# Kernel optimization log

Hardware: AMD Instinct MI355X
Metric: run time of the kernel (lower is better)

The kernel has to match this reference:

```python
import jax, jax.numpy as jnp
import numpy as np
from jax import lax

B, T = 64, 512
VOCAB, E = 16000, 128
USCRIPT, UE = 64, 16
F, MAX_NGRAM = 128, 5
C = 13  # num_classes


def setup_inputs() -> dict:
    key = jax.random.key(0)
    ks = jax.random.split(key, 18)
    inp = {
        "input_char": jax.random.randint(ks[0], (B, T), 0, VOCAB),
        "input_script": jax.random.randint(ks[1], (B, T), 0, USCRIPT),
        "input_mask": jnp.ones((B, T), dtype=bool),
        "char_emb": jax.random.normal(ks[2], (VOCAB, E), jnp.float32) * 0.02,
        "uscript_emb": jax.random.normal(ks[3], (USCRIPT, UE), jnp.float32) * 0.02,
        "dense_w": jax.random.normal(ks[4], (MAX_NGRAM * F + UE, C), jnp.float32) * 0.05,
        "dense_b": jnp.zeros((C,), jnp.float32),
        "trans": jax.random.normal(ks[5], (C, C), jnp.float32) * 0.1,
        "left_b": jax.random.normal(ks[6], (C,), jnp.float32) * 0.1,
        "right_b": jax.random.normal(ks[7], (C,), jnp.float32) * 0.1,
    }
    for i in range(1, MAX_NGRAM + 1):
        inp[f"conv_w{i}"] = jax.random.normal(ks[7 + i], (i, E, F), jnp.float32) * (1.0 / np.sqrt(i * E))
        inp[f"conv_b{i}"] = jnp.zeros((F,), jnp.float32)
    return inp


def _conv1d_same_relu(x, w, b):
    # x: [B,T,Cin], w: [K,Cin,Cout]
    y = lax.conv_general_dilated(x, w, window_strides=(1,), padding="SAME",
                                 dimension_numbers=("NWC", "WIO", "NWC"))
    return jax.nn.relu(y + b)


def _potentials(input_char, input_script, input_mask, char_emb, uscript_emb,
                conv_ws, conv_bs, dense_w, dense_b, left_b, right_b):
    emb = char_emb[input_char]              # [B,T,E]
    uemb = uscript_emb[input_script]        # [B,T,UE]
    feats = [_conv1d_same_relu(emb, w, b) for w, b in zip(conv_ws, conv_bs)]
    ctx = jnp.concatenate(feats + [uemb], axis=-1)          # [B,T,5F+UE]
    pot = jnp.einsum("btf,fc->btc", ctx, dense_w) + dense_b  # [B,T,C]
    # boundary energies (tfa CRF use_boundary=True): add left_b at first
    # valid step, right_b at last valid step per the mask
    m = input_mask.astype(pot.dtype)[..., None]              # [B,T,1]
    prev_m = jnp.pad(m[:, :-1], ((0, 0), (1, 0), (0, 0)))
    next_m = jnp.pad(m[:, 1:], ((0, 0), (0, 1), (0, 0)))
    pot = pot + m * (1.0 - prev_m) * left_b + m * (1.0 - next_m) * right_b
    return pot


def _viterbi_decode(pot, trans):
    # pot: [B,T,C], trans: [C,C]; full-length sequences (mask all ones)
    def fwd(state, pot_t):
        scores = state[:, :, None] + trans[None]   # [B, prev, cur]
        bp = jnp.argmax(scores, axis=1)            # [B,C]
        state = jnp.max(scores, axis=1) + pot_t    # [B,C]
        return state, bp

    final, bps = lax.scan(fwd, pot[:, 0], jnp.swapaxes(pot[:, 1:], 0, 1))
    last = jnp.argmax(final, axis=-1)              # [B]

    def back(tag, bp_t):
        prev = jnp.take_along_axis(bp_t, tag[:, None], axis=1)[:, 0]
        return prev, prev

    _, tags = lax.scan(back, last, bps, reverse=True)  # [T-1, B], forward order
    decoded = jnp.concatenate([jnp.swapaxes(tags, 0, 1), last[:, None]], axis=1)
    return decoded.astype(jnp.int32)


def reference(input_char, input_script, input_mask, char_emb, uscript_emb,
              conv_w1, conv_b1, conv_w2, conv_b2, conv_w3, conv_b3,
              conv_w4, conv_b4, conv_w5, conv_b5,
              dense_w, dense_b, trans, left_b, right_b):
    conv_ws = [conv_w1, conv_w2, conv_w3, conv_w4, conv_w5]
    conv_bs = [conv_b1, conv_b2, conv_b3, conv_b4, conv_b5]
    pot = _potentials(input_char, input_script, input_mask, char_emb, uscript_emb,
                      conv_ws, conv_bs, dense_w, dense_b, left_b, right_b)
    seq_len = jnp.sum(input_mask.astype(jnp.int32), axis=1)
    decoded = _viterbi_decode(pot, trans)
    return decoded, pot, seq_len, trans
```

## Files before the change

kernel.cpp:

```cpp
#include <hip/hip_runtime.h>

#define NB 64
#define NT 512
#define NC 13
#define AP 136
#define WP 72
#define PT 516
#define USTRIDE 18432
#define DWT_H   552960
#define DWT_L   563200
#define WS_NEED 1146880
#define WS_SROWS 1146880
#define WS_NEED2 (WS_SROWS + NB*NT*16*4)

typedef short s8v __attribute__((ext_vector_type(8)));
typedef float f4v __attribute__((ext_vector_type(4)));
typedef unsigned short ush;
typedef unsigned int u32;

__device__ __forceinline__ ush f2bf(float f){
    union { float f; u32 u; } v; v.f = f;
    u32 r = v.u + 0x7fffu + ((v.u >> 16) & 1u);
    return (ush)(r >> 16);
}
__device__ __forceinline__ float bf2f(ush h){
    union { u32 u; float f; } v; v.u = ((u32)h) << 16; return v.f;
}

__global__ __launch_bounds__(512)
void prep_kernel(const float* __restrict__ cw1, const float* __restrict__ cw2,
                 const float* __restrict__ cw3, const float* __restrict__ cw4,
                 const float* __restrict__ cw5, const float* __restrict__ dense_w,
                 ush* __restrict__ ws)
{
    int bx = blockIdx.x, tid = threadIdx.x;
    if (bx < 30) {
        int u = bx, ut = u >> 1, eh = u & 1;
        int fb = ut<1?0: ut<3?1: ut<6?2: ut<10?3:4;
        int jj = ut - fb*(fb+1)/2;
        const float* cw = fb==0?cw1: fb==1?cw2: fb==2?cw3: fb==3?cw4: cw5;
        #pragma unroll
        for (int it = 0; it < 2; ++it) {
            int g = it*512 + tid;
            int f = g & 127;
            int e8 = (g >> 7) << 3;
            float v[8];
            #pragma unroll
            for (int q = 0; q < 8; ++q)
                v[q] = cw[(jj*128 + eh*64 + e8 + q)*128 + f];
            ush h8[8], l8[8];
            #pragma unroll
            for (int q = 0; q < 8; ++q) {
                h8[q] = f2bf(v[q]);
                l8[q] = f2bf(v[q] - bf2f(h8[q]));
            }
            uint4 hv, lv;
            hv.x = h8[0] | ((u32)h8[1]<<16); hv.y = h8[2] | ((u32)h8[3]<<16);
            hv.z = h8[4] | ((u32)h8[5]<<16); hv.w = h8[6] | ((u32)h8[7]<<16);
            lv.x = l8[0] | ((u32)l8[1]<<16); lv.y = l8[2] | ((u32)l8[3]<<16);
            lv.z = l8[4] | ((u32)l8[5]<<16); lv.w = l8[6] | ((u32)l8[7]<<16);
            *(uint4*)&ws[u*USTRIDE + f*WP + e8]        = hv;
            *(uint4*)&ws[u*USTRIDE + 9216 + f*WP + e8] = lv;
        }
    } else {
        int fb = bx - 30;
        #pragma unroll
        for (int it = 0; it < 4; ++it) {
            int idx = it*512 + tid;
            int c = idx >> 7, f = idx & 127;
            float v = (c < 13) ? dense_w[(fb*128 + f)*13 + c] : 0.f;
            ush hi = f2bf(v);
            ws[DWT_H + fb*2048 + idx] = hi;
            ws[DWT_L + fb*2048 + idx] = f2bf(v - bf2f(hi));
        }
    }
}

__global__ __launch_bounds__(512)
void pot_kernel_ws(const int* __restrict__ input_char,
                   const int* __restrict__ input_script,
                   const float* __restrict__ char_emb,
                   const float* __restrict__ uscript_emb,
                   const float* __restrict__ dense_w,
                   const float* __restrict__ dense_b,
                   const float* __restrict__ left_b,
                   const float* __restrict__ right_b,
                   const float* __restrict__ cb1, const float* __restrict__ cb2,
                   const float* __restrict__ cb3, const float* __restrict__ cb4,
                   const float* __restrict__ cb5,
                   const ush* __restrict__ ws,
                   float* __restrict__ out_pot)
{
    __shared__ __align__(16) ush smem[77280];
    ush* Ah     = smem;
    ush* Al     = smem + 17952;
    ush* feat_h = smem + 54336;
    ush* feat_l = smem + 63040;
    float* uebt = (float*)(smem + 72768);
    float* dwue = (float*)(smem + 76864);

    const int tid  = threadIdx.x;
    const int lane = tid & 63;
    const int wid  = tid >> 6;
    const int tg   = wid >> 2;
    const int fg   = wid & 3;
    const int lr   = lane & 15;
    const int lq   = lane >> 4;
    const int bb   = blockIdx.x >> 2;
    const int t0   = (blockIdx.x & 3) << 7;

    {
        const char* g = (const char*)ws;
        char* l = (char*)(smem + 35904);
        #pragma unroll
        for (int i = 0; i < 5; ++i) {
            int idx = wid + (i << 3);
            if (i < 4 || wid < 4)
                __builtin_amdgcn_global_load_lds(
                    (const __attribute__((address_space(1))) void*)(g + idx*1024 + lane*16),
                    (__attribute__((address_space(3))) void*)(l + idx*1024 + lane*16), 16, 0, 0);
        }
    }

    for (int i = tid; i < 132*16; i += 512) {
        int row = i >> 4, s = (i & 15) << 3;
        int t = t0 + row - 2;
        uint4 hv = {0,0,0,0}, lv = {0,0,0,0};
        if (t >= 0 && t < NT) {
            int ch = input_char[bb*NT + t];
            const float* src = char_emb + ch*128 + s;
            float4 x0 = *(const float4*)src;
            float4 x1 = *(const float4*)(src + 4);
            float fs[8] = {x0.x,x0.y,x0.z,x0.w,x1.x,x1.y,x1.z,x1.w};
            ush h[8], l[8];
            #pragma unroll
            for (int q = 0; q < 8; ++q) {
                h[q] = f2bf(fs[q]);
                l[q] = f2bf(fs[q] - bf2f(h[q]));
            }
            hv.x = h[0] | ((u32)h[1]<<16); hv.y = h[2] | ((u32)h[3]<<16);
            hv.z = h[4] | ((u32)h[5]<<16); hv.w = h[6] | ((u32)h[7]<<16);
            lv.x = l[0] | ((u32)l[1]<<16); lv.y = l[2] | ((u32)l[3]<<16);
            lv.z = l[4] | ((u32)l[5]<<16); lv.w = l[6] | ((u32)l[7]<<16);
        }
        *(uint4*)&Ah[row*AP + s] = hv;
        *(uint4*)&Al[row*AP + s] = lv;
    }
    for (int i = tid; i < 2048; i += 512) {
        int uu = i >> 7, tl = i & 127;
        uebt[uu*128 + tl] = uscript_emb[input_script[bb*NT + t0 + tl]*16 + uu];
    }
    if (tid < 208) dwue[tid] = dense_w[640*13 + tid];
    __syncthreads();

    const float* cbs[5] = {cb1, cb2, cb3, cb4, cb5};

    f4v cacc[4][2];
    #pragma unroll
    for (int mt = 0; mt < 4; ++mt)
        #pragma unroll
        for (int nt = 0; nt < 2; ++nt) cacc[mt][nt] = (f4v){0.f,0.f,0.f,0.f};
    f4v dacc = (f4v){0.f,0.f,0.f,0.f};

    #pragma unroll 1
    for (int u = 0; u < 30; ++u) {
        int ut  = u >> 1, eh = u & 1;
        int fb  = ut<1?0: ut<3?1: ut<6?2: ut<10?3:4;
        int jj  = ut - fb*(fb+1)/2;
        int jsh = (2 - (fb >> 1)) + jj;

        if (u < 29) {
            const char* g = (const char*)ws + (u + 1)*36864;
            char* l = (char*)(smem + (((u + 1) & 1) ? 54336 : 35904));
            #pragma unroll
            for (int i = 0; i < 5; ++i) {
                int idx = wid + (i << 3);
                if (i < 4 || wid < 4)
                    __builtin_amdgcn_global_load_lds(
                        (const __attribute__((address_space(1))) void*)(g + idx*1024 + lane*16),
                        (__attribute__((address_space(3))) void*)(l + idx*1024 + lane*16), 16, 0, 0);
            }
        }

        const ush* Wh = smem + ((u & 1) ? 54336 : 35904);
        const ush* Wl = Wh + 9216;
        #pragma unroll
        for (int kk = 0; kk < 2; ++kk) {
            int ko = kk*32 + (lq << 3);
            s8v bh[2], bl[2];
            #pragma unroll
            for (int nt = 0; nt < 2; ++nt) {
                int frow = fg*32 + nt*16 + lr;
                bh[nt] = *(const s8v*)&Wh[frow*WP + ko];
                bl[nt] = *(const s8v*)&Wl[frow*WP + ko];
            }
            #pragma unroll
            for (int mt = 0; mt < 4; ++mt) {
                int row = tg*64 + mt*16 + lr + jsh;
                int ai  = row*AP + eh*64 + ko;
                s8v ah = *(const s8v*)&Ah[ai];
                s8v al = *(const s8v*)&Al[ai];
                #pragma unroll
                for (int nt = 0; nt < 2; ++nt) {
                    cacc[mt][nt] = __builtin_amdgcn_mfma_f32_16x16x32_bf16(ah, bh[nt], cacc[mt][nt], 0,0,0);
                    cacc[mt][nt] = __builtin_amdgcn_mfma_f32_16x16x32_bf16(ah, bl[nt], cacc[mt][nt], 0,0,0);
                    cacc[mt][nt] = __builtin_amdgcn_mfma_f32_16x16x32_bf16(al, bh[nt], cacc[mt][nt], 0,0,0);
                }
            }
        }

        if (u == 1 || u == 5 || u == 11 || u == 19 || u == 29) {
            __syncthreads();
            float cbv0 = cbs[fb][fg*32 + lr];
            float cbv1 = cbs[fb][fg*32 + 16 + lr];

            #pragma unroll 1
            for (int h = 0; h < 2; ++h) {
                if (tg == h) {
                    #pragma unroll
                    for (int mt = 0; mt < 4; ++mt)
                        #pragma unroll
                        for (int nt = 0; nt < 2; ++nt)
                            #pragma unroll
                            for (int r = 0; r < 4; ++r) {
                                float v = fmaxf(cacc[mt][nt][r] + (nt ? cbv1 : cbv0), 0.f);
                                int rw = mt*16 + (lq << 2) + r;
                                int f  = fg*32 + nt*16 + lr;
                                ush hh = f2bf(v);
                                feat_h[rw*AP + f] = hh;
                                feat_l[rw*AP + f] = f2bf(v - bf2f(hh));
                            }
                }
                __syncthreads();
                if (tg == h) {
                    int trow = fg*16 + lr;
                    #pragma unroll
                    for (int kf = 0; kf < 4; ++kf) {
                        int f0 = kf*32 + (lq << 3);
                        s8v a2h = *(const s8v*)&ws[DWT_H + fb*2048 + lr*128 + f0];
                        s8v a2l = *(const s8v*)&ws[DWT_L + fb*2048 + lr*128 + f0];
                        s8v b2h = *(const s8v*)&feat_h[trow*AP + f0];
                        s8v b2l = *(const s8v*)&feat_l[trow*AP + f0];
                        dacc = __builtin_amdgcn_mfma_f32_16x16x32_bf16(a2h, b2h, dacc, 0,0,0);
                        dacc = __builtin_amdgcn_mfma_f32_16x16x32_bf16(a2h, b2l, dacc, 0,0,0);
                        dacc = __builtin_amdgcn_mfma_f32_16x16x32_bf16(a2l, b2h, dacc, 0,0,0);
                    }
                    if (fb == 4) {
                        int tloc  = tg*64 + fg*16 + lr;
                        int tglob = t0 + tloc;
                        float pc[4];
                        #pragma unroll
                        for (int r = 0; r < 4; ++r) pc[r] = dacc[r];
                        #pragma unroll
                        for (int uu = 0; uu < 16; ++uu) {
                            float uv = uebt[uu*128 + tloc];
                            #pragma unroll
                            for (int r = 0; r < 4; ++r) {
                                int c = (lq << 2) + r;
                                if (c < 13) pc[r] = fmaf(uv, dwue[uu*13 + c], pc[r]);
                            }
                        }
                        #pragma unroll
                        for (int r = 0; r < 4; ++r) {
                            int c = (lq << 2) + r;
                            if (c < 13) {
                                float v = pc[r] + dense_b[c];
                                if (tglob == 0)    v += left_b[c];
                                if (tglob == NT-1) v += right_b[c];
                                out_pot[(bb*NT + tglob)*13 + c] = v;
                            }
                        }
                    }
                }
                __syncthreads();
            }
            #pragma unroll
            for (int mt = 0; mt < 4; ++mt)
                #pragma unroll
                for (int nt = 0; nt < 2; ++nt) cacc[mt][nt] = (f4v){0.f,0.f,0.f,0.f};
        } else {
            __syncthreads();
        }
    }
}

__global__ __launch_bounds__(512)
void pot_kernel_fb(const int* __restrict__ input_char,
                   const int* __restrict__ input_script,
                   const float* __restrict__ char_emb,
                   const float* __restrict__ uscript_emb,
                   const float* __restrict__ dense_w,
                   const float* __restrict__ dense_b,
                   const float* __restrict__ left_b,
                   const float* __restrict__ right_b,
                   const float* __restrict__ cw1, const float* __restrict__ cb1,
                   const float* __restrict__ cw2, const float* __restrict__ cb2,
                   const float* __restrict__ cw3, const float* __restrict__ cb3,
                   const float* __restrict__ cw4, const float* __restrict__ cb4,
                   const float* __restrict__ cw5, const float* __restrict__ cb5,
                   float* __restrict__ out_pot)
{
    __shared__ __align__(16) ush smem[71744];
    ush* Ah     = smem;
    ush* Al     = smem + 17952;
    ush* Wh     = smem + 35904;
    ush* Wl     = smem + 45120;
    ush* feat_h = smem + 54336;
    ush* feat_l = smem + 63040;
    float* dwlds = (float*)(smem + 35904);
    float* dwue  = (float*)(smem + 39232);
    float* uebt  = (float*)(smem + 39648);

    const int tid  = threadIdx.x;
    const int lane = tid & 63;
    const int wid  = tid >> 6;
    const int tg   = wid >> 2;
    const int fg   = wid & 3;
    const int lr   = lane & 15;
    const int lq   = lane >> 4;
    const int bb   = blockIdx.x >> 2;
    const int t0   = (blockIdx.x & 3) << 7;

    for (int i = tid; i < 132*16; i += 512) {
        int row = i >> 4, s = (i & 15) << 3;
        int t = t0 + row - 2;
        uint4 hv = {0,0,0,0}, lv = {0,0,0,0};
        if (t >= 0 && t < NT) {
            int ch = input_char[bb*NT + t];
            const float* src = char_emb + ch*128 + s;
            float4 x0 = *(const float4*)src;
            float4 x1 = *(const float4*)(src + 4);
            float fs[8] = {x0.x,x0.y,x0.z,x0.w,x1.x,x1.y,x1.z,x1.w};
            ush h[8], l[8];
            #pragma unroll
            for (int q = 0; q < 8; ++q) {
                h[q] = f2bf(fs[q]);
                l[q] = f2bf(fs[q] - bf2f(h[q]));
            }
            hv.x = h[0] | ((u32)h[1]<<16); hv.y = h[2] | ((u32)h[3]<<16);
            hv.z = h[4] | ((u32)h[5]<<16); hv.w = h[6] | ((u32)h[7]<<16);
            lv.x = l[0] | ((u32)l[1]<<16); lv.y = l[2] | ((u32)l[3]<<16);
            lv.z = l[4] | ((u32)l[5]<<16); lv.w = l[6] | ((u32)l[7]<<16);
        }
        *(uint4*)&Ah[row*AP + s] = hv;
        *(uint4*)&Al[row*AP + s] = lv;
    }

    const float* cws[5] = {cw1, cw2, cw3, cw4, cw5};
    const float* cbs[5] = {cb1, cb2, cb3, cb4, cb5};

    f4v cacc[4][2];
    #pragma unroll
    for (int mt = 0; mt < 4; ++mt)
        #pragma unroll
        for (int nt = 0; nt < 2; ++nt) cacc[mt][nt] = (f4v){0.f,0.f,0.f,0.f};
    f4v dacc = (f4v){0.f,0.f,0.f,0.f};

    #pragma unroll 1
    for (int u = 0; u < 30; ++u) {
        int ut  = u >> 1, eh = u & 1;
        int fb  = ut<1?0: ut<3?1: ut<6?2: ut<10?3:4;
        int jj  = ut - fb*(fb+1)/2;
        int jsh = (2 - (fb >> 1)) + jj;
        const float* cw = cws[fb] + (jj*128 + eh*64)*128;

        __syncthreads();
        for (int g = tid; g < 1024; g += 512) {
            int f = g & 127, e8 = (g >> 7) << 3;
            float v[8];
            #pragma unroll
            for (int q = 0; q < 8; ++q) v[q] = cw[(e8 + q)*128 + f];
            ush h8[8], l8[8];
            #pragma unroll
            for (int q = 0; q < 8; ++q) {
                h8[q] = f2bf(v[q]);
                l8[q] = f2bf(v[q] - bf2f(h8[q]));
            }
            uint4 hv, lv;
            hv.x = h8[0] | ((u32)h8[1]<<16); hv.y = h8[2] | ((u32)h8[3]<<16);
            hv.z = h8[4] | ((u32)h8[5]<<16); hv.w = h8[6] | ((u32)h8[7]<<16);
            lv.x = l8[0] | ((u32)l8[1]<<16); lv.y = l8[2] | ((u32)l8[3]<<16);
            lv.z = l8[4] | ((u32)l8[5]<<16); lv.w = l8[6] | ((u32)l8[7]<<16);
            *(uint4*)&Wh[f*WP + e8] = hv;
            *(uint4*)&Wl[f*WP + e8] = lv;
        }
        __syncthreads();

        #pragma unroll
        for (int kk = 0; kk < 2; ++kk) {
            int ko = kk*32 + (lq << 3);
            s8v bh[2], bl[2];
            #pragma unroll
            for (int nt = 0; nt < 2; ++nt) {
                int frow = fg*32 + nt*16 + lr;
                bh[nt] = *(const s8v*)&Wh[frow*WP + ko];
                bl[nt] = *(const s8v*)&Wl[frow*WP + ko];
            }
            #pragma unroll
            for (int mt = 0; mt < 4; ++mt) {
                int row = tg*64 + mt*16 + lr + jsh;
                int ai  = row*AP + eh*64 + ko;
                s8v ah = *(const s8v*)&Ah[ai];
                s8v al = *(const s8v*)&Al[ai];
                #pragma unroll
                for (int nt = 0; nt < 2; ++nt) {
                    cacc[mt][nt] = __builtin_amdgcn_mfma_f32_16x16x32_bf16(ah, bh[nt], cacc[mt][nt], 0,0,0);
                    cacc[mt][nt] = __builtin_amdgcn_mfma_f32_16x16x32_bf16(ah, bl[nt], cacc[mt][nt], 0,0,0);
                    cacc[mt][nt] = __builtin_amdgcn_mfma_f32_16x16x32_bf16(al, bh[nt], cacc[mt][nt], 0,0,0);
                }
            }
        }

        if (u == 1 || u == 5 || u == 11 || u == 19 || u == 29) {
            __syncthreads();
            for (int i = tid; i < 128*13; i += 512)
                dwlds[i] = dense_w[fb*128*13 + i];
            if (fb == 4) {
                for (int i = tid; i < 16*13; i += 512)
                    dwue[i] = dense_w[640*13 + i];
                for (int i = tid; i < 2048; i += 512) {
                    int uu = i >> 7, tl = i & 127;
                    uebt[uu*128 + tl] = uscript_emb[input_script[bb*NT + t0 + tl]*16 + uu];
                }
            }
            __syncthreads();

            float cbv0 = cbs[fb][fg*32 + lr];
            float cbv1 = cbs[fb][fg*32 + 16 + lr];

            #pragma unroll 1
            for (int h = 0; h < 2; ++h) {
                if (tg == h) {
                    #pragma unroll
                    for (int mt = 0; mt < 4; ++mt)
                        #pragma unroll
                        for (int nt = 0; nt < 2; ++nt)
                            #pragma unroll
                            for (int r = 0; r < 4; ++r) {
                                float v = fmaxf(cacc[mt][nt][r] + (nt ? cbv1 : cbv0), 0.f);
                                int rw = mt*16 + (lq << 2) + r;
                                int f  = fg*32 + nt*16 + lr;
                                ush hh = f2bf(v);
                                feat_h[rw*AP + f] = hh;
                                feat_l[rw*AP + f] = f2bf(v - bf2f(hh));
                            }
                }
                __syncthreads();
                if (tg == h) {
                    int trow = fg*16 + lr;
                    #pragma unroll
                    for (int kf = 0; kf < 4; ++kf) {
                        int f0 = kf*32 + (lq << 3);
                        float dv[8];
                        #pragma unroll
                        for (int q = 0; q < 8; ++q) dv[q] = dwlds[(f0 + q)*13 + lr];
                        s8v a2h, a2l;
                        #pragma unroll
                        for (int q = 0; q < 8; ++q) {
                            ush hh = f2bf(dv[q]);
                            a2h[q] = (short)hh;
                            a2l[q] = (short)f2bf(dv[q] - bf2f(hh));
                        }
                        s8v b2h = *(const s8v*)&feat_h[trow*AP + f0];
                        s8v b2l = *(const s8v*)&feat_l[trow*AP + f0];
                        dacc = __builtin_amdgcn_mfma_f32_16x16x32_bf16(a2h, b2h, dacc, 0,0,0);
                        dacc = __builtin_amdgcn_mfma_f32_16x16x32_bf16(a2h, b2l, dacc, 0,0,0);
                        dacc = __builtin_amdgcn_mfma_f32_16x16x32_bf16(a2l, b2h, dacc, 0,0,0);
                    }
                    if (fb == 4) {
                        int tloc  = tg*64 + fg*16 + lr;
                        int tglob = t0 + tloc;
                        float pc[4];
                        #pragma unroll
                        for (int r = 0; r < 4; ++r) pc[r] = dacc[r];
                        #pragma unroll
                        for (int uu = 0; uu < 16; ++uu) {
                            float uv = uebt[uu*128 + tloc];
                            #pragma unroll
                            for (int r = 0; r < 4; ++r) {
                                int c = (lq << 2) + r;
                                if (c < 13) pc[r] = fmaf(uv, dwue[uu*13 + c], pc[r]);
                            }
                        }
                        #pragma unroll
                        for (int r = 0; r < 4; ++r) {
                            int c = (lq << 2) + r;
                            if (c < 13) {
                                float v = pc[r] + dense_b[c];
                                if (tglob == 0)    v += left_b[c];
                                if (tglob == NT-1) v += right_b[c];
                                out_pot[(bb*NT + tglob)*13 + c] = v;
                            }
                        }
                    }
                }
                __syncthreads();
            }
            #pragma unroll
            for (int mt = 0; mt < 4; ++mt)
                #pragma unroll
                for (int nt = 0; nt < 2; ++nt) cacc[mt][nt] = (f4v){0.f,0.f,0.f,0.f};
        }
    }
}

#define DPPF(dst, src, ctrl) \
    dst = __int_as_float(__builtin_amdgcn_mov_dpp(__float_as_int(src), ctrl, 0xF, 0xF, false))

__global__ __launch_bounds__(256)
void scan_kernel(const float* __restrict__ pot,
                 const float* __restrict__ trans,
                 float* __restrict__ srows)
{
    __shared__ __align__(16) float ptld[16 * PT];
    __shared__ float t_lds[NC * NC];

    const int b   = blockIdx.x;
    const int tid = threadIdx.x;

    for (int i = tid; i < 3 * PT; i += 256) ptld[13 * PT + i] = 0.f;
    for (int i = tid; i < NT * NC; i += 256) {
        int t = i / NC, c = i - t * NC;
        ptld[c * PT + t] = pot[b * NT * NC + i];
    }
    for (int i = tid; i < NC * NC; i += 256) t_lds[i] = trans[i];
    __syncthreads();

    if (tid >= 16) return;
    const int c = tid;
    int r1 = __builtin_amdgcn_mov_dpp(c, 0x121, 0xF, 0xF, false);
    const bool fwd = (r1 == ((c + 1) & 15));
    float tc[16];
    #pragma unroll
    for (int k = 0; k < 16; ++k) {
        int p = fwd ? ((c + k) & 15) : ((c - k) & 15);
        tc[k] = (c < 13 && p < 13) ? t_lds[p * NC + c] : -1e30f;
    }
    float s = (c < 13) ? ptld[c * PT] : -1e30f;
    float* srb = srows + b * NT * 16;
    srb[c] = s;
    int t = 1;

    auto step = [&](float pv) {
        float v0 = s, v1, v2, v3, v4, v5, v6, v7;
        float v8, v9, v10, v11, v12, v13, v14, v15;
        DPPF(v1, v0, 0x121);
        DPPF(v2, v0, 0x122); DPPF(v3, v1, 0x122);
        DPPF(v4, v0, 0x124); DPPF(v5, v1, 0x124);
        DPPF(v6, v2, 0x124); DPPF(v7, v3, 0x124);
        DPPF(v8,  v0, 0x128); DPPF(v9,  v1, 0x128);
        DPPF(v10, v2, 0x128); DPPF(v11, v3, 0x128);
        DPPF(v12, v4, 0x128); DPPF(v13, v5, 0x128);
        DPPF(v14, v6, 0x128); DPPF(v15, v7, 0x128);
        float m0 = fmaxf(v0  + tc[0],  v1  + tc[1]);
        float m1 = fmaxf(v2  + tc[2],  v3  + tc[3]);
        float m2 = fmaxf(v4  + tc[4],  v5  + tc[5]);
        float m3 = fmaxf(v6  + tc[6],  v7  + tc[7]);
        float m4 = fmaxf(v8  + tc[8],  v9  + tc[9]);
        float m5 = fmaxf(v10 + tc[10], v11 + tc[11]);
        float m6 = fmaxf(v12 + tc[12], v13 + tc[13]);
        float m7 = fmaxf(v14 + tc[14], v15 + tc[15]);
        float n0 = fmaxf(m0, m1), n1 = fmaxf(m2, m3);
        float n2 = fmaxf(m4, m5), n3 = fmaxf(m6, m7);
        s = fmaxf(fmaxf(n0, n1), fmaxf(n2, n3)) + pv;
        srb[t * 16 + c] = s;
        ++t;
    };

    const float* prow = &ptld[c * PT];
    float4 pvv = *(const float4*)&prow[4];
    step(prow[1]);
    step(prow[2]);
    step(prow[3]);
    #pragma unroll 1
    for (int t4 = 4; t4 < NT; t4 += 4) {
        float4 cur = pvv;
        if (t4 + 4 < NT) pvv = *(const float4*)&prow[t4 + 4];
        step(cur.x); step(cur.y); step(cur.z); step(cur.w);
    }
}

__global__ __launch_bounds__(256)
void backtrack_kernel(const float* __restrict__ srows,
                      const float* __restrict__ trans,
                      float* __restrict__ out_dec,
                      float* __restrict__ out_seq,
                      float* __restrict__ out_trans)
{
    __shared__ __align__(16) float sl[NT * 16];
    __shared__ float t_lds[NC * NC];
    __shared__ unsigned char path_lds[16 * 13 * 32];
    __shared__ unsigned char entry_lds[16 * 13];
    __shared__ int chunk_e[16];

    const int b   = blockIdx.x;
    const int tid = threadIdx.x;

    {
        const float4* src = reinterpret_cast<const float4*>(srows + b * NT * 16);
        float4* dst = reinterpret_cast<float4*>(sl);
        for (int i = tid; i < NT * 16 / 4; i += 256) dst[i] = src[i];
        for (int i = tid; i < NC * NC; i += 256) t_lds[i] = trans[i];
    }
    __syncthreads();

    if (tid < 16 * 13) {
        const int chunk = tid / 13;
        const int e     = tid - chunk * 13;
        unsigned char* path = &path_lds[(chunk * 13 + e) * 32];
        int cur = e;
        path[31] = (unsigned char)e;
        for (int tl = 31; tl >= 1; --tl) {
            const float* srow = &sl[(chunk * 32 + tl - 1) * 16];
            float best = -1e30f; int bi = 0;
            #pragma unroll
            for (int p = 0; p < NC; ++p) {
                float v = srow[p] + t_lds[p * NC + cur];
                if (v > best) { best = v; bi = p; }
            }
            cur = bi;
            path[tl - 1] = (unsigned char)cur;
        }
        if (chunk > 0) {
            const float* srow = &sl[(chunk * 32 - 1) * 16];
            float best = -1e30f; int bi = 0;
            #pragma unroll
            for (int p = 0; p < NC; ++p) {
                float v = srow[p] + t_lds[p * NC + cur];
                if (v > best) { best = v; bi = p; }
            }
            entry_lds[chunk * 13 + e] = (unsigned char)bi;
        }
    }
    __syncthreads();

    if (tid == 0) {
        float best = -1e30f; int last = 0;
        for (int c = 0; c < NC; ++c) {
            float v = sl[(NT - 1) * 16 + c];
            if (v > best) { best = v; last = c; }
        }
        chunk_e[15] = last;
        for (int i = 15; i >= 1; --i)
            chunk_e[i - 1] = entry_lds[i * 13 + chunk_e[i]];
    }
    __syncthreads();

    float* dec = out_dec + b * NT;
    for (int t = tid; t < NT; t += 256) {
        int ck = t >> 5;
        dec[t] = (float)path_lds[(ck * 13 + chunk_e[ck]) * 32 + (t & 31)];
    }
    if (tid == 0) out_seq[b] = (float)NT;
    if (b == 0) {
        for (int i = tid; i < NC * NC; i += 256) out_trans[i] = trans[i];
    }
}

__global__ __launch_bounds__(256)
void viterbi_mono(const float* __restrict__ pot,
                  const float* __restrict__ trans,
                  float* __restrict__ out_dec,
                  float* __restrict__ out_seq,
                  float* __restrict__ out_trans)
{
    __shared__ __align__(16) float s_lds[NT * NC];
    __shared__ __align__(16) float ptld[16 * PT];
    __shared__ float t_lds[NC * NC];
    __shared__ unsigned char path_lds[16 * 13 * 32];
    __shared__ unsigned char entry_lds[16 * 13];
    __shared__ int chunk_e[16];

    const int b   = blockIdx.x;
    const int tid = threadIdx.x;

    for (int i = tid; i < 3 * PT; i += 256) ptld[13 * PT + i] = 0.f;
    for (int i = tid; i < NT * NC; i += 256) {
        int t = i / NC, c = i - t * NC;
        float v = pot[b * NT * NC + i];
        ptld[c * PT + t] = v;
        if (t == 0) s_lds[c] = v;
    }
    for (int i = tid; i < NC * NC; i += 256) t_lds[i] = trans[i];
    __syncthreads();

    if (tid < 16) {
        const int c = tid;
        int r1 = __builtin_amdgcn_mov_dpp(c, 0x121, 0xF, 0xF, false);
        const bool fwd = (r1 == ((c + 1) & 15));
        float tc[16];
        #pragma unroll
        for (int k = 0; k < 16; ++k) {
            int p = fwd ? ((c + k) & 15) : ((c - k) & 15);
            tc[k] = (c < 13 && p < 13) ? t_lds[p * NC + c] : -1e30f;
        }
        float s = (c < 13) ? s_lds[c] : -1e30f;
        int t = 1;

        auto step = [&](float pv) {
            float v0 = s, v1, v2, v3, v4, v5, v6, v7;
            float v8, v9, v10, v11, v12, v13, v14, v15;
            DPPF(v1, v0, 0x121);
            DPPF(v2, v0, 0x122); DPPF(v3, v1, 0x122);
            DPPF(v4, v0, 0x124); DPPF(v5, v1, 0x124);
            DPPF(v6, v2, 0x124); DPPF(v7, v3, 0x124);
            DPPF(v8,  v0, 0x128); DPPF(v9,  v1, 0x128);
            DPPF(v10, v2, 0x128); DPPF(v11, v3, 0x128);
            DPPF(v12, v4, 0x128); DPPF(v13, v5, 0x128);
            DPPF(v14, v6, 0x128); DPPF(v15, v7, 0x128);
            float m0 = fmaxf(v0  + tc[0],  v1  + tc[1]);
            float m1 = fmaxf(v2  + tc[2],  v3  + tc[3]);
            float m2 = fmaxf(v4  + tc[4],  v5  + tc[5]);
            float m3 = fmaxf(v6  + tc[6],  v7  + tc[7]);
            float m4 = fmaxf(v8  + tc[8],  v9  + tc[9]);
            float m5 = fmaxf(v10 + tc[10], v11 + tc[11]);
            float m6 = fmaxf(v12 + tc[12], v13 + tc[13]);
            float m7 = fmaxf(v14 + tc[14], v15 + tc[15]);
            float n0 = fmaxf(m0, m1), n1 = fmaxf(m2, m3);
            float n2 = fmaxf(m4, m5), n3 = fmaxf(m6, m7);
            s = fmaxf(fmaxf(n0, n1), fmaxf(n2, n3)) + pv;
            if (c < 13) s_lds[t * NC + c] = s;
            ++t;
        };

        const float* prow = &ptld[c * PT];
        float4 pvv = *(const float4*)&prow[4];
        step(prow[1]);
        step(prow[2]);
        step(prow[3]);
        #pragma unroll 1
        for (int t4 = 4; t4 < NT; t4 += 4) {
            float4 cur = pvv;
            if (t4 + 4 < NT) pvv = *(const float4*)&prow[t4 + 4];
            step(cur.x); step(cur.y); step(cur.z); step(cur.w);
        }
    }
    __syncthreads();

    if (tid < 16 * 13) {
        const int chunk = tid / 13;
        const int e     = tid - chunk * 13;
        unsigned char* path = &path_lds[(chunk * 13 + e) * 32];
        int cur = e;
        path[31] = (unsigned char)e;
        for (int tl = 31; tl >= 1; --tl) {
            const float* srow = &s_lds[(chunk * 32 + tl - 1) * NC];
            float best = -1e30f; int bi = 0;
            #pragma unroll
            for (int p = 0; p < NC; ++p) {
                float v = srow[p] + t_lds[p * NC + cur];
                if (v > best) { best = v; bi = p; }
            }
            cur = bi;
            path[tl - 1] = (unsigned char)cur;
        }
        if (chunk > 0) {
            const float* srow = &s_lds[(chunk * 32 - 1) * NC];
            float best = -1e30f; int bi = 0;
            #pragma unroll
            for (int p = 0; p < NC; ++p) {
                float v = srow[p] + t_lds[p * NC + cur];
                if (v > best) { best = v; bi = p; }
            }
            entry_lds[chunk * 13 + e] = (unsigned char)bi;
        }
    }
    __syncthreads();

    if (tid == 0) {
        float best = -1e30f; int last = 0;
        for (int c = 0; c < NC; ++c) {
            float v = s_lds[(NT - 1) * NC + c];
            if (v > best) { best = v; last = c; }
        }
        chunk_e[15] = last;
        for (int i = 15; i >= 1; --i)
            chunk_e[i - 1] = entry_lds[i * 13 + chunk_e[i]];
    }
    __syncthreads();

    float* dec = out_dec + b * NT;
    for (int t = tid; t < NT; t += 256) {
        int ck = t >> 5;
        dec[t] = (float)path_lds[(ck * 13 + chunk_e[ck]) * 32 + (t & 31)];
    }
    if (tid == 0) out_seq[b] = (float)NT;
    if (b == 0) {
        for (int i = tid; i < NC * NC; i += 256) out_trans[i] = trans[i];
    }
}

extern "C" void kernel_launch(void* const* d_in, const int* in_sizes, int n_in,
                              void* d_out, int out_size, void* d_ws, size_t ws_size,
                              hipStream_t stream) {
    const int*   input_char   = (const int*)d_in[0];
    const int*   input_script = (const int*)d_in[1];
    const float* char_emb     = (const float*)d_in[3];
    const float* uscript_emb  = (const float*)d_in[4];
    const float* dense_w      = (const float*)d_in[5];
    const float* dense_b      = (const float*)d_in[6];
    const float* trans        = (const float*)d_in[7];
    const float* left_b       = (const float*)d_in[8];
    const float* right_b      = (const float*)d_in[9];
    const float* cw1 = (const float*)d_in[10];
    const float* cb1 = (const float*)d_in[11];
    const float* cw2 = (const float*)d_in[12];
    const float* cb2 = (const float*)d_in[13];
    const float* cw3 = (const float*)d_in[14];
    const float* cb3 = (const float*)d_in[15];
    const float* cw4 = (const float*)d_in[16];
    const float* cb4 = (const float*)d_in[17];
    const float* cw5 = (const float*)d_in[18];
    const float* cb5 = (const float*)d_in[19];

    float* out       = (float*)d_out;
    float* out_dec   = out;
    float* out_pot   = out + NB * NT;
    float* out_seq   = out_pot + NB * NT * NC;
    float* out_trans = out_seq + NB;

    bool have_prep = ws_size >= (size_t)WS_NEED;
    bool have_srow = ws_size >= (size_t)WS_NEED2;

    if (have_prep) {
        hipLaunchKernelGGL(prep_kernel, dim3(35), dim3(512), 0, stream,
                           cw1, cw2, cw3, cw4, cw5, dense_w, (ush*)d_ws);
        hipLaunchKernelGGL(pot_kernel_ws, dim3(256), dim3(512), 0, stream,
                           input_char, input_script, char_emb, uscript_emb,
                           dense_w, dense_b, left_b, right_b,
                           cb1, cb2, cb3, cb4, cb5,
                           (const ush*)d_ws, out_pot);
    } else {
        hipLaunchKernelGGL(pot_kernel_fb, dim3(256), dim3(512), 0, stream,
                           input_char, input_script, char_emb, uscript_emb,
                           dense_w, dense_b, left_b, right_b,
                           cw1, cb1, cw2, cb2, cw3, cb3, cw4, cb4, cw5, cb5,
                           out_pot);
    }

    if (have_srow) {
        float* srows = (float*)((char*)d_ws + WS_SROWS);
        hipLaunchKernelGGL(scan_kernel, dim3(NB), dim3(256), 0, stream,
                           out_pot, trans, srows);
        hipLaunchKernelGGL(backtrack_kernel, dim3(NB), dim3(256), 0, stream,
                           srows, trans, out_dec, out_seq, out_trans);
    } else {
        hipLaunchKernelGGL(viterbi_mono, dim3(NB), dim3(256), 0, stream,
                           out_pot, trans, out_dec, out_seq, out_trans);
    }
}
```

Measured before the change: 158.2 us.

## Halve pot kernel block to 256 threads with wider per-wave N tiles

Shrinks the potentials kernel from 8 to 4 waves per block. Each wave now computes a 64x64 conv output tile (4x4 MFMA accumulators instead of 4x2), so every A fragment loaded from LDS is reused across twice as many MFMAs. The weight-tile prefetch and the dense-projection step are rewritten for 4 waves: all waves now take part in each half's dense MFMA, with separate accumulators per half. The cost is more accumulator registers per thread and fewer waves to hide latency, since the large LDS footprint already limits the kernel to one block per CU.

```diff
diff --git a/kernel.cpp b/kernel.cpp
--- a/kernel.cpp
+++ b/kernel.cpp
@@ -76,7 +76,7 @@
     }
 }
 
-__global__ __launch_bounds__(512)
+__global__ __launch_bounds__(256)
 void pot_kernel_ws(const int* __restrict__ input_char,
                    const int* __restrict__ input_script,
                    const float* __restrict__ char_emb,
@@ -102,27 +102,28 @@
     const int tid  = threadIdx.x;
     const int lane = tid & 63;
     const int wid  = tid >> 6;
-    const int tg   = wid >> 2;
-    const int fg   = wid & 3;
+    const int tg   = wid >> 1;
+    const int fg   = wid & 1;
     const int lr   = lane & 15;
     const int lq   = lane >> 4;
     const int bb   = blockIdx.x >> 2;
     const int t0   = (blockIdx.x & 3) << 7;
 
-    {
-        const char* g = (const char*)ws;
-        char* l = (char*)(smem + 35904);
+    auto issue_unit = [&](int u) {
+        const char* g = (const char*)ws + u * 36864;
+        char* l = (char*)(smem + ((u & 1) ? 54336 : 35904));
         #pragma unroll
-        for (int i = 0; i < 5; ++i) {
-            int idx = wid + (i << 3);
-            if (i < 4 || wid < 4)
-                __builtin_amdgcn_global_load_lds(
-                    (const __attribute__((address_space(1))) void*)(g + idx*1024 + lane*16),
-                    (__attribute__((address_space(3))) void*)(l + idx*1024 + lane*16), 16, 0, 0);
-        }
-    }
-
-    for (int i = tid; i < 132*16; i += 512) {
+        for (int i = 0; i < 9; ++i) {
+            int off = (wid + (i << 2)) * 1024 + lane * 16;
+            __builtin_amdgcn_global_load_lds(
+                (const __attribute__((address_space(1))) void*)(g + off),
+                (__attribute__((address_space(3))) void*)(l + off), 16, 0, 0);
+        }
+    };
+
+    issue_unit(0);
+
+    for (int i = tid; i < 132*16; i += 256) {
         int row = i >> 4, s = (i & 15) << 3;
         int t = t0 + row - 2;
         uint4 hv = {0,0,0,0}, lv = {0,0,0,0};
@@ -146,7 +147,7 @@
         *(uint4*)&Ah[row*AP + s] = hv;
         *(uint4*)&Al[row*AP + s] = lv;
     }
-    for (int i = tid; i < 2048; i += 512) {
+    for (int i = tid; i < 2048; i += 256) {
         int uu = i >> 7, tl = i & 127;
         uebt[uu*128 + tl] = uscript_emb[input_script[bb*NT + t0 + tl]*16 + uu];
     }
@@ -155,12 +156,76 @@
 
     const float* cbs[5] = {cb1, cb2, cb3, cb4, cb5};
 
-    f4v cacc[4][2];
+    f4v cacc[4][4];
     #pragma unroll
     for (int mt = 0; mt < 4; ++mt)
         #pragma unroll
-        for (int nt = 0; nt < 2; ++nt) cacc[mt][nt] = (f4v){0.f,0.f,0.f,0.f};
-    f4v dacc = (f4v){0.f,0.f,0.f,0.f};
+        for (int nt = 0; nt < 4; ++nt) cacc[mt][nt] = (f4v){0.f,0.f,0.f,0.f};
+    f4v dacc0 = (f4v){0.f,0.f,0.f,0.f};
+    f4v dacc1 = (f4v){0.f,0.f,0.f,0.f};
+
+    auto dense_half = [&](int h, f4v& dacc, int fb) {
+        float cbv[4];
+        #pragma unroll
+        for (int nt = 0; nt < 4; ++nt) cbv[nt] = cbs[fb][fg*64 + nt*16 + lr];
+        if (tg == h) {
+            #pragma unroll
+            for (int mt = 0; mt < 4; ++mt)
+                #pragma unroll
+                for (int nt = 0; nt < 4; ++nt)
+                    #pragma unroll
+                    for (int r = 0; r < 4; ++r) {
+                        float v = fmaxf(cacc[mt][nt][r] + cbv[nt], 0.f);
+                        int rw = mt*16 + (lq << 2) + r;
+                        int f  = fg*64 + nt*16 + lr;
+                        ush hh = f2bf(v);
+                        feat_h[rw*AP + f] = hh;
+                        feat_l[rw*AP + f] = f2bf(v - bf2f(hh));
+                    }
+        }
+        __syncthreads();
+        {
+            int trow = wid*16 + lr;
+            #pragma unroll
+            for (int kf = 0; kf < 4; ++kf) {
+                int f0 = kf*32 + (lq << 3);
+                s8v a2h = *(const s8v*)&ws[DWT_H + fb*2048 + lr*128 + f0];
+                s8v a2l = *(const s8v*)&ws[DWT_L + fb*2048 + lr*128 + f0];
+                s8v b2h = *(const s8v*)&feat_h[trow*AP + f0];
+                s8v b2l = *(const s8v*)&feat_l[trow*AP + f0];
+                dacc = __builtin_amdgcn_mfma_f32_16x16x32_bf16(a2h, b2h, dacc, 0,0,0);
+                dacc = __builtin_amdgcn_mfma_f32_16x16x32_bf16(a2h, b2l, dacc, 0,0,0);
+                dacc = __builtin_amdgcn_mfma_f32_16x16x32_bf16(a2l, b2h, dacc, 0,0,0);
+            }
+            if (fb == 4) {
+                int tloc  = h*64 + wid*16 + lr;
+                int tglob = t0 + tloc;
+                float pc[4];
+                #pragma unroll
+                for (int r = 0; r < 4; ++r) pc[r] = dacc[r];
+                #pragma unroll
+                for (int uu = 0; uu < 16; ++uu) {
+                    float uv = uebt[uu*128 + tloc];
+                    #pragma unroll
+                    for (int r = 0; r < 4; ++r) {
+                        int c = (lq << 2) + r;
+                        if (c < 13) pc[r] = fmaf(uv, dwue[uu*13 + c], pc[r]);
+                    }
+                }
+                #pragma unroll
+                for (int r = 0; r < 4; ++r) {
+                    int c = (lq << 2) + r;
+                    if (c < 13) {
+                        float v = pc[r] + dense_b[c];
+                        if (tglob == 0)    v += left_b[c];
+                        if (tglob == NT-1) v += right_b[c];
+                        out_pot[(bb*NT + tglob)*13 + c] = v;
+                    }
+                }
+            }
+        }
+        __syncthreads();
+    };
 
     #pragma unroll 1
     for (int u = 0; u < 30; ++u) {
@@ -169,28 +234,17 @@
         int jj  = ut - fb*(fb+1)/2;
         int jsh = (2 - (fb >> 1)) + jj;
 
-        if (u < 29) {
-            const char* g = (const char*)ws + (u + 1)*36864;
-            char* l = (char*)(smem + (((u + 1) & 1) ? 54336 : 35904));
-            #pragma unroll
-            for (int i = 0; i < 5; ++i) {
-                int idx = wid + (i << 3);
-                if (i < 4 || wid < 4)
-                    __builtin_amdgcn_global_load_lds(
-                        (const __attribute__((address_space(1))) void*)(g + idx*1024 + lane*16),
-                        (__attribute__((address_space(3))) void*)(l + idx*1024 + lane*16), 16, 0, 0);
-            }
-        }
+        if (u < 29) issue_unit(u + 1);
 
         const ush* Wh = smem + ((u & 1) ? 54336 : 35904);
         const ush* Wl = Wh + 9216;
         #pragma unroll
         for (int kk = 0; kk < 2; ++kk) {
             int ko = kk*32 + (lq << 3);
-            s8v bh[2], bl[2];
-            #pragma unroll
-            for (int nt = 0; nt < 2; ++nt) {
-                int frow = fg*32 + nt*16 + lr;
+            s8v bh[4], bl[4];
+            #pragma unroll
+            for (int nt = 0; nt < 4; ++nt) {
+                int frow = fg*64 + nt*16 + lr;
                 bh[nt] = *(const s8v*)&Wh[frow*WP + ko];
                 bl[nt] = *(const s8v*)&Wl[frow*WP + ko];
             }
@@ -201,7 +255,7 @@
                 s8v ah = *(const s8v*)&Ah[ai];
                 s8v al = *(const s8v*)&Al[ai];
                 #pragma unroll
-                for (int nt = 0; nt < 2; ++nt) {
+                for (int nt = 0; nt < 4; ++nt) {
                     cacc[mt][nt] = __builtin_amdgcn_mfma_f32_16x16x32_bf16(ah, bh[nt], cacc[mt][nt], 0,0,0);
                     cacc[mt][nt] = __builtin_amdgcn_mfma_f32_16x16x32_bf16(ah, bl[nt], cacc[mt][nt], 0,0,0);
                     cacc[mt][nt] = __builtin_amdgcn_mfma_f32_16x16x32_bf16(al, bh[nt], cacc[mt][nt], 0,0,0);
@@ -211,73 +265,12 @@
 
         if (u == 1 || u == 5 || u == 11 || u == 19 || u == 29) {
             __syncthreads();
-            float cbv0 = cbs[fb][fg*32 + lr];
-            float cbv1 = cbs[fb][fg*32 + 16 + lr];
-
-            #pragma unroll 1
-            for (int h = 0; h < 2; ++h) {
-                if (tg == h) {
-                    #pragma unroll
-                    for (int mt = 0; mt < 4; ++mt)
-                        #pragma unroll
-                        for (int nt = 0; nt < 2; ++nt)
-                            #pragma unroll
-                            for (int r = 0; r < 4; ++r) {
-                                float v = fmaxf(cacc[mt][nt][r] + (nt ? cbv1 : cbv0), 0.f);
-                                int rw = mt*16 + (lq << 2) + r;
-                                int f  = fg*32 + nt*16 + lr;
-                                ush hh = f2bf(v);
-                                feat_h[rw*AP + f] = hh;
-                                feat_l[rw*AP + f] = f2bf(v - bf2f(hh));
-                            }
-                }
-                __syncthreads();
-                if (tg == h) {
-                    int trow = fg*16 + lr;
-                    #pragma unroll
-                    for (int kf = 0; kf < 4; ++kf) {
-                        int f0 = kf*32 + (lq << 3);
-                        s8v a2h = *(const s8v*)&ws[DWT_H + fb*2048 + lr*128 + f0];
-                        s8v a2l = *(const s8v*)&ws[DWT_L + fb*2048 + lr*128 + f0];
-                        s8v b2h = *(const s8v*)&feat_h[trow*AP + f0];
-                        s8v b2l = *(const s8v*)&feat_l[trow*AP + f0];
-                        dacc = __builtin_amdgcn_mfma_f32_16x16x32_bf16(a2h, b2h, dacc, 0,0,0);
-                        dacc = __builtin_amdgcn_mfma_f32_16x16x32_bf16(a2h, b2l, dacc, 0,0,0);
-                        dacc = __builtin_amdgcn_mfma_f32_16x16x32_bf16(a2l, b2h, dacc, 0,0,0);
-                    }
-                    if (fb == 4) {
-                        int tloc  = tg*64 + fg*16 + lr;
-                        int tglob = t0 + tloc;
-                        float pc[4];
-                        #pragma unroll
-                        for (int r = 0; r < 4; ++r) pc[r] = dacc[r];
-                        #pragma unroll
-                        for (int uu = 0; uu < 16; ++uu) {
-                            float uv = uebt[uu*128 + tloc];
-                            #pragma unroll
-                            for (int r = 0; r < 4; ++r) {
-                                int c = (lq << 2) + r;
-                                if (c < 13) pc[r] = fmaf(uv, dwue[uu*13 + c], pc[r]);
-                            }
-                        }
-                        #pragma unroll
-                        for (int r = 0; r < 4; ++r) {
-                            int c = (lq << 2) + r;
-                            if (c < 13) {
-                                float v = pc[r] + dense_b[c];
-                                if (tglob == 0)    v += left_b[c];
-                                if (tglob == NT-1) v += right_b[c];
-                                out_pot[(bb*NT + tglob)*13 + c] = v;
-                            }
-                        }
-                    }
-                }
-                __syncthreads();
-            }
+            dense_half(0, dacc0, fb);
+            dense_half(1, dacc1, fb);
             #pragma unroll
             for (int mt = 0; mt < 4; ++mt)
                 #pragma unroll
-                for (int nt = 0; nt < 2; ++nt) cacc[mt][nt] = (f4v){0.f,0.f,0.f,0.f};
+                for (int nt = 0; nt < 4; ++nt) cacc[mt][nt] = (f4v){0.f,0.f,0.f,0.f};
         } else {
             __syncthreads();
         }
@@ -801,7 +794,7 @@
     const float* dense_b      = (const float*)d_in[6];
     const float* trans        = (const float*)d_in[7];
     const float* left_b       = (const float*)d_in[8];
-    const float* right_b      = (const float*)d_in[9];
+    const float* right_b     = (const float*)d_in[9];
     const float* cw1 = (const float*)d_in[10];
     const float* cb1 = (const float*)d_in[11];
     const float* cw2 = (const float*)d_in[12];
@@ -825,7 +818,7 @@
     if (have_prep) {
         hipLaunchKernelGGL(prep_kernel, dim3(35), dim3(512), 0, stream,
                            cw1, cw2, cw3, cw4, cw5, dense_w, (ush*)d_ws);
-        hipLaunchKernelGGL(pot_kernel_ws, dim3(256), dim3(512), 0, stream,
+        hipLaunchKernelGGL(pot_kernel_ws, dim3(256), dim3(256), 0, stream,
                            input_char, input_script, char_emb, uscript_emb,
                            dense_w, dense_b, left_b, right_b,
                            cb1, cb2, cb3, cb4, cb5,
```

After: 179.0 us. +13.2%, slower.
